# Performance work log

Measured on AMD Instinct MI355X. Metric: run time of the kernel, lower is better.

The kernel has to match this reference:

```python
import jax, jax.numpy as jnp
import numpy as np

B = 16384        # batch
P = 8            # num policies (experts)
D = 512          # latent dim
A = 64           # action dim
H = 1024         # hidden dim


def setup_inputs() -> dict:
    key = jax.random.key(0)
    ks = jax.random.split(key, 7)
    latents = jax.random.normal(ks[0], (B, D), dtype=jnp.float32)
    actions = jax.random.normal(ks[1], (B, A), dtype=jnp.float32)
    policy_indices = jax.random.randint(ks[2], (B,), 0, P, dtype=jnp.int64)
    # Per-policy 2-layer MLP params: concat(latent, action) -> hidden -> latent
    scale1 = 1.0 / np.sqrt(D + A)
    scale2 = 1.0 / np.sqrt(H)
    W1 = jax.random.normal(ks[3], (P, D + A, H), dtype=jnp.float32) * scale1
    b1 = jnp.zeros((P, H), dtype=jnp.float32)
    W2 = jax.random.normal(ks[4], (P, H, D), dtype=jnp.float32) * scale2
    b2 = jnp.zeros((P, D), dtype=jnp.float32)
    return {"latents": latents, "actions": actions, "policy_indices": policy_indices,
            "W1": W1, "b1": b1, "W2": W2, "b2": b2}


def reference(latents, actions, policy_indices, W1, b1, W2, b2):
    # Original: for each policy i, route rows with policy_indices == i through
    # that policy's dynamics model; scatter results back into next_latents.
    # Equivalent dense form: run all experts, then select per-row expert output.
    x = jnp.concatenate([latents, actions], axis=-1)          # [B, D+A]
    h = jax.nn.relu(jnp.einsum('bd,pdh->bph', x, W1) + b1)    # [B, P, H]
    y = jnp.einsum('bph,phd->bpd', h, W2) + b2                # [B, P, D]
    idx = policy_indices[:, None, None]                       # [B, 1, 1]
    next_latents = jnp.take_along_axis(y, idx, axis=1)[:, 0]  # [B, D]
    return next_latents
```

## Files before the change

kernel.cpp:

```cpp
#include <hip/hip_runtime.h>
#include <hip/hip_bf16.h>
#include <stdint.h>

#define B_SZ 16384
#define P_SZ 8
#define D_SZ 512
#define A_SZ 64
#define K1 576
#define H_SZ 1024
#define NSEG 64
#define MB_MAX 72
#define BPAD (B_SZ + P_SZ*256)
#define PREP_BLOCKS (BPAD * 72 / 256)
#define TRANS_BLOCKS (32 * 32 * 16)

typedef __bf16 bf16_t;
typedef __bf16 bf16x8 __attribute__((ext_vector_type(8)));
typedef float f32x4 __attribute__((ext_vector_type(4)));

__device__ __forceinline__ void glds16(const void* g, void* l) {
    __builtin_amdgcn_global_load_lds(
        (const __attribute__((address_space(1))) unsigned*)g,
        (__attribute__((address_space(3))) unsigned*)l, 16, 0, 0);
}


__global__ __launch_bounds__(256) void hist_block(const int* __restrict__ pol,
                                                  int* __restrict__ blockhist,
                                                  int* __restrict__ rowidx) {
    __shared__ int lc[P_SZ];
    int t = threadIdx.x;
    if (t < P_SZ) lc[t] = 0;
    __syncthreads();
    int gid = blockIdx.x * 256 + t;
    rowidx[gid] = -1;
    if (gid < BPAD - B_SZ) rowidx[B_SZ + gid] = -1;
    atomicAdd(&lc[pol[gid]], 1);
    __syncthreads();
    if (t < P_SZ) blockhist[blockIdx.x * P_SZ + t] = lc[t];
}

__global__ __launch_bounds__(64) void prefix_kernel(const int* __restrict__ blockhist,
                                                    int* __restrict__ counts,
                                                    int* __restrict__ cursors,
                                                    int* __restrict__ blk_p) {
    int t = threadIdx.x;
    if (t < P_SZ) {
        int s = 0;
        for (int b = 0; b < NSEG; ++b) s += blockhist[b * P_SZ + t];
        counts[t] = s;
    }
    __syncthreads();
    if (t == 0) {
        int run = 0;
        for (int p = 0; p < P_SZ; ++p) {
            cursors[p] = run;
            int nb = (counts[p] + 255) >> 8;
            for (int b = 0; b < nb; ++b) blk_p[(run >> 8) + b] = p;
            run += nb * 256;
        }
        for (int b = run >> 8; b < MB_MAX; ++b) blk_p[b] = -1;
    }
}

__global__ __launch_bounds__(256) void scatter_agg(const int* __restrict__ pol,
                                                   int* __restrict__ cursors,
                                                   int* __restrict__ rowidx) {
    __shared__ int lc[P_SZ], base_s[P_SZ];
    int t = threadIdx.x;
    if (t < P_SZ) lc[t] = 0;
    __syncthreads();
    int i = blockIdx.x * 256 + t;
    int p = pol[i];
    int lpos = atomicAdd(&lc[p], 1);
    __syncthreads();
    if (t < P_SZ) base_s[t] = atomicAdd(&cursors[t], lc[t]);
    __syncthreads();
    rowidx[base_s[p] + lpos] = i;
}


__global__ __launch_bounds__(256) void prep_all(const float* __restrict__ latents,
                                                const float* __restrict__ actions,
                                                const int* __restrict__ rowidx,
                                                const float* __restrict__ W1,
                                                const float* __restrict__ W2,
                                                bf16_t* __restrict__ xs,
                                                bf16_t* __restrict__ w1t,
                                                bf16_t* __restrict__ w2t) {
    int bx = blockIdx.x;
    int tid = threadIdx.x;
    if (bx < PREP_BLOCKS) {
        int idx = bx * 256 + tid;
        int s = idx / 72;
        int col = (idx - s * 72) * 8;
        int g = rowidx[s];
        bf16x8 o;
        if (g < 0) {
            o = (bf16x8){0,0,0,0,0,0,0,0};
        } else {
            const float* src;
            if (col < D_SZ) src = latents + (size_t)g * D_SZ + col;
            else            src = actions + (size_t)g * A_SZ + (col - D_SZ);
            f32x4 v0 = *(const f32x4*)src;
            f32x4 v1 = *(const f32x4*)(src + 4);
            o[0] = (bf16_t)v0[0]; o[1] = (bf16_t)v0[1]; o[2] = (bf16_t)v0[2]; o[3] = (bf16_t)v0[3];
            o[4] = (bf16_t)v1[0]; o[5] = (bf16_t)v1[1]; o[6] = (bf16_t)v1[2]; o[7] = (bf16_t)v1[3];
        }
        *(bf16x8*)(xs + (size_t)s * K1 + col) = o;
        return;
    }
    int tz = bx - PREP_BLOCKS;
    int z = tz >> 10;
    int rem = tz & 1023;
    int k0 = (rem & 31) * 32, n0 = (rem >> 5) * 32;
    int K = (z < P_SZ) ? K1 : H_SZ;
    int N = (z < P_SZ) ? H_SZ : D_SZ;
    if (k0 >= K || n0 >= N) return;
    int p = z & 7;
    const float* Wp = ((z < P_SZ) ? W1 : W2) + (size_t)p * K * N;
    bf16_t* WTp = ((z < P_SZ) ? w1t : w2t) + (size_t)p * N * K;
    __shared__ float ls[32][33];
#pragma unroll
    for (int e = 0; e < 4; ++e) {
        int idx = e * 256 + tid;
        int kk = idx >> 5, nn = idx & 31;
        ls[kk][nn] = Wp[(size_t)(k0 + kk) * N + n0 + nn];
    }
    __syncthreads();
#pragma unroll
    for (int e = 0; e < 2; ++e) {
        int idx = e * 256 + tid;
        int nn = idx >> 4, kp = (idx & 15) * 2;
        union { bf16_t h[2]; unsigned u; } pk;
        pk.h[0] = (bf16_t)ls[kp][nn];
        pk.h[1] = (bf16_t)ls[kp + 1][nn];
        *(unsigned*)&WTp[(size_t)(n0 + nn) * K + k0 + kp] = pk.u;
    }
}


__global__ __launch_bounds__(256, 2) void gemm1_kernel(
    const bf16_t* __restrict__ xs, const bf16_t* __restrict__ w1t,
    const float* __restrict__ b1, const int* __restrict__ blk_p,
    bf16_t* __restrict__ h) {

    const int p = blk_p[blockIdx.x];
    if (p < 0) return;
    const int m0 = blockIdx.x * 256;
    const int n0 = blockIdx.y * 128;

    __shared__ __align__(16) bf16_t As[256 * 32];
    __shared__ __align__(16) bf16_t Bs[128 * 32];

    const int tid = threadIdx.x;
    const int wave = tid >> 6, lane = tid & 63;

    const bf16_t* a_src[4]; bf16_t* a_dst[4];
#pragma unroll
    for (int i = 0; i < 4; ++i) {
        int c = (wave * 4 + i) * 64 + lane;
        int r = c >> 2;
        int kl = (c & 3) ^ ((r >> 1) & 3);
        a_src[i] = xs + (size_t)(m0 + r) * K1 + kl * 8;
        a_dst[i] = As + c * 8;
    }
    const bf16_t* b_src[2]; bf16_t* b_dst[2];
#pragma unroll
    for (int i = 0; i < 2; ++i) {
        int c = (wave * 2 + i) * 64 + lane;
        int r = c >> 2;
        int kl = (c & 3) ^ ((r >> 1) & 3);
        b_src[i] = w1t + ((size_t)p * H_SZ + n0 + r) * K1 + kl * 8;
        b_dst[i] = Bs + c * 8;
    }

    const int l16 = lane & 15, qd = lane >> 4;
    const int swz = (l16 >> 1) & 3;
    int aoff[4], boff[8];
#pragma unroll
    for (int i = 0; i < 4; ++i) aoff[i] = (wave * 64 + i * 16 + l16) * 32 + ((qd ^ swz) * 8);
#pragma unroll
    for (int j = 0; j < 8; ++j) boff[j] = (j * 16 + l16) * 32 + ((qd ^ swz) * 8);

    f32x4 acc[4][8];
#pragma unroll
    for (int i = 0; i < 4; ++i)
#pragma unroll
        for (int j = 0; j < 8; ++j)
            acc[i][j] = (f32x4){0.f, 0.f, 0.f, 0.f};

    for (int kt = 0; kt < K1; kt += 32) {
        __syncthreads();
#pragma unroll
        for (int i = 0; i < 4; ++i) glds16(a_src[i] + kt, a_dst[i]);
#pragma unroll
        for (int i = 0; i < 2; ++i) glds16(b_src[i] + kt, b_dst[i]);
        __syncthreads();
        bf16x8 af[4], bfv[8];
#pragma unroll
        for (int i = 0; i < 4; ++i) af[i] = *(const bf16x8*)(As + aoff[i]);
#pragma unroll
        for (int j = 0; j < 8; ++j) bfv[j] = *(const bf16x8*)(Bs + boff[j]);
#pragma unroll
        for (int i = 0; i < 4; ++i)
#pragma unroll
            for (int j = 0; j < 8; ++j)
                acc[i][j] = __builtin_amdgcn_mfma_f32_16x16x32_bf16(af[i], bfv[j], acc[i][j], 0, 0, 0);
    }

#pragma unroll
    for (int i = 0; i < 4; ++i) {
#pragma unroll
        for (int r = 0; r < 4; ++r) {
            int ml = wave * 64 + i * 16 + qd * 4 + r;
            size_t row = (size_t)(m0 + ml);
#pragma unroll
            for (int j = 0; j < 8; ++j) {
                int n = n0 + j * 16 + l16;
                float v = acc[i][j][r] + b1[p * H_SZ + n];
                h[row * H_SZ + n] = (bf16_t)fmaxf(v, 0.f);
            }
        }
    }
}

__global__ __launch_bounds__(256, 2) void gemm2_kernel(
    const bf16_t* __restrict__ h, const bf16_t* __restrict__ w2t,
    const float* __restrict__ b2, const int* __restrict__ blk_p,
    const int* __restrict__ rowidx, float* __restrict__ out) {

    const int p = blk_p[blockIdx.x];
    if (p < 0) return;
    const int m0 = blockIdx.x * 256;
    const int n0 = blockIdx.y * 64;

    __shared__ __align__(16) bf16_t As[256 * 32];
    __shared__ __align__(16) bf16_t Bs[64 * 32];

    const int tid = threadIdx.x;
    const int wave = tid >> 6, lane = tid & 63;

    const bf16_t* a_src[4]; bf16_t* a_dst[4];
#pragma unroll
    for (int i = 0; i < 4; ++i) {
        int c = (wave * 4 + i) * 64 + lane;
        int r = c >> 2;
        int kl = (c & 3) ^ ((r >> 1) & 3);
        a_src[i] = h + (size_t)(m0 + r) * H_SZ + kl * 8;
        a_dst[i] = As + c * 8;
    }
    const bf16_t* b_src0; bf16_t* b_dst0;
    {
        int c = wave * 64 + lane;
        int r = c >> 2;
        int kl = (c & 3) ^ ((r >> 1) & 3);
        b_src0 = w2t + ((size_t)p * D_SZ + n0 + r) * H_SZ + kl * 8;
        b_dst0 = Bs + c * 8;
    }

    const int l16 = lane & 15, qd = lane >> 4;
    const int swz = (l16 >> 1) & 3;
    int aoff[4], boff[4];
#pragma unroll
    for (int i = 0; i < 4; ++i) aoff[i] = (wave * 64 + i * 16 + l16) * 32 + ((qd ^ swz) * 8);
#pragma unroll
    for (int j = 0; j < 4; ++j) boff[j] = (j * 16 + l16) * 32 + ((qd ^ swz) * 8);

    f32x4 acc[4][4];
#pragma unroll
    for (int i = 0; i < 4; ++i)
#pragma unroll
        for (int j = 0; j < 4; ++j)
            acc[i][j] = (f32x4){0.f, 0.f, 0.f, 0.f};

    for (int kt = 0; kt < H_SZ; kt += 32) {
        __syncthreads();
#pragma unroll
        for (int i = 0; i < 4; ++i) glds16(a_src[i] + kt, a_dst[i]);
        glds16(b_src0 + kt, b_dst0);
        __syncthreads();
        bf16x8 af[4], bfv[4];
#pragma unroll
        for (int i = 0; i < 4; ++i) af[i] = *(const bf16x8*)(As + aoff[i]);
#pragma unroll
        for (int j = 0; j < 4; ++j) bfv[j] = *(const bf16x8*)(Bs + boff[j]);
#pragma unroll
        for (int i = 0; i < 4; ++i)
#pragma unroll
            for (int j = 0; j < 4; ++j)
                acc[i][j] = __builtin_amdgcn_mfma_f32_16x16x32_bf16(af[i], bfv[j], acc[i][j], 0, 0, 0);
    }

#pragma unroll
    for (int i = 0; i < 4; ++i) {
#pragma unroll
        for (int r = 0; r < 4; ++r) {
            int ml = wave * 64 + i * 16 + qd * 4 + r;
            int g = rowidx[m0 + ml];
            if (g >= 0) {
                size_t orow = (size_t)g * D_SZ;
#pragma unroll
                for (int j = 0; j < 4; ++j) {
                    int n = n0 + j * 16 + l16;
                    out[orow + n] = acc[i][j][r] + b2[p * D_SZ + n];
                }
            }
        }
    }
}


extern "C" void kernel_launch(void* const* d_in, const int* in_sizes, int n_in,
                              void* d_out, int out_size, void* d_ws, size_t ws_size,
                              hipStream_t stream) {
    const float* latents = (const float*)d_in[0];
    const float* actions = (const float*)d_in[1];
    const int*   pol     = (const int*)d_in[2];
    const float* W1      = (const float*)d_in[3];
    const float* b1      = (const float*)d_in[4];
    const float* W2      = (const float*)d_in[5];
    const float* b2      = (const float*)d_in[6];
    float* out = (float*)d_out;

    char* ws = (char*)d_ws;
    int* counts    = (int*)ws;
    int* cursors   = counts + P_SZ;
    int* blk_p     = cursors + P_SZ;
    int* blockhist = blk_p + MB_MAX;
    int* rowidx    = blockhist + NSEG * P_SZ;
    size_t pos = ((size_t)(2 * P_SZ + MB_MAX + NSEG * P_SZ + BPAD) * sizeof(int) + 255) & ~(size_t)255;
    bf16_t* xs  = (bf16_t*)(ws + pos);  pos += (size_t)BPAD * K1 * 2;
    bf16_t* hbuf= (bf16_t*)(ws + pos);  pos += (size_t)BPAD * H_SZ * 2;
    bf16_t* w1t = (bf16_t*)(ws + pos);  pos += (size_t)P_SZ * H_SZ * K1 * 2;
    bf16_t* w2t = (bf16_t*)(ws + pos);  pos += (size_t)P_SZ * D_SZ * H_SZ * 2;

    hist_block<<<NSEG, 256, 0, stream>>>(pol, blockhist, rowidx);
    prefix_kernel<<<1, 64, 0, stream>>>(blockhist, counts, cursors, blk_p);
    scatter_agg<<<NSEG, 256, 0, stream>>>(pol, cursors, rowidx);
    prep_all<<<PREP_BLOCKS + TRANS_BLOCKS, 256, 0, stream>>>(
        latents, actions, rowidx, W1, W2, xs, w1t, w2t);
    gemm1_kernel<<<dim3(MB_MAX, H_SZ / 128), 256, 0, stream>>>(xs, w1t, b1, blk_p, hbuf);
    gemm2_kernel<<<dim3(MB_MAX, D_SZ / 64), 256, 0, stream>>>(hbuf, w2t, b2, blk_p, rowidx, out);
}
```

Measured before the change: 210.8 us.

## Double-buffer LDS tiles in both GEMMs and vectorize weight transpose loads

Both grouped GEMM kernels now keep two LDS buffers for the A and B tiles. The next K-tile is issued with global_load_lds before the current one is consumed, leaving a single barrier per iteration. The goal is to hide global-load latency behind the MFMA work. Occupancy hints are raised to 3 and 4 blocks per CU to go with the larger LDS footprint. The prep transpose now reads weights as float4 instead of scalars. The compiler may still insert full vmcnt waits before the LDS reads, which would limit the overlap, and the higher launch bounds constrain register allocation.

```diff
diff --git a/kernel.cpp b/kernel.cpp
--- a/kernel.cpp
+++ b/kernel.cpp
@@ -121,11 +121,13 @@
     const float* Wp = ((z < P_SZ) ? W1 : W2) + (size_t)p * K * N;
     bf16_t* WTp = ((z < P_SZ) ? w1t : w2t) + (size_t)p * N * K;
     __shared__ float ls[32][33];
-#pragma unroll
-    for (int e = 0; e < 4; ++e) {
-        int idx = e * 256 + tid;
-        int kk = idx >> 5, nn = idx & 31;
-        ls[kk][nn] = Wp[(size_t)(k0 + kk) * N + n0 + nn];
+    {
+        int kk = tid >> 3, nn = (tid & 7) * 4;
+        f32x4 v = *(const f32x4*)&Wp[(size_t)(k0 + kk) * N + n0 + nn];
+        ls[kk][nn]     = v[0];
+        ls[kk][nn + 1] = v[1];
+        ls[kk][nn + 2] = v[2];
+        ls[kk][nn + 3] = v[3];
     }
     __syncthreads();
 #pragma unroll
@@ -140,7 +142,7 @@
 }
 
 
-__global__ __launch_bounds__(256, 2) void gemm1_kernel(
+__global__ __launch_bounds__(256, 3) void gemm1_kernel(
     const bf16_t* __restrict__ xs, const bf16_t* __restrict__ w1t,
     const float* __restrict__ b1, const int* __restrict__ blk_p,
     bf16_t* __restrict__ h) {
@@ -150,8 +152,10 @@
     const int m0 = blockIdx.x * 256;
     const int n0 = blockIdx.y * 128;
 
-    __shared__ __align__(16) bf16_t As[256 * 32];
-    __shared__ __align__(16) bf16_t Bs[128 * 32];
+    constexpr int AE = 256 * 32;
+    constexpr int BE = 128 * 32;
+    __shared__ __align__(16) bf16_t As[2 * AE];
+    __shared__ __align__(16) bf16_t Bs[2 * BE];
 
     const int tid = threadIdx.x;
     const int wave = tid >> 6, lane = tid & 63;
@@ -175,6 +179,11 @@
         b_dst[i] = Bs + c * 8;
     }
 
+#pragma unroll
+    for (int i = 0; i < 4; ++i) glds16(a_src[i], a_dst[i]);
+#pragma unroll
+    for (int i = 0; i < 2; ++i) glds16(b_src[i], b_dst[i]);
+
     const int l16 = lane & 15, qd = lane >> 4;
     const int swz = (l16 >> 1) & 3;
     int aoff[4], boff[8];
@@ -190,18 +199,25 @@
         for (int j = 0; j < 8; ++j)
             acc[i][j] = (f32x4){0.f, 0.f, 0.f, 0.f};
 
-    for (int kt = 0; kt < K1; kt += 32) {
+    constexpr int NT = K1 / 32;
+    for (int t = 0; t < NT; ++t) {
         __syncthreads();
-#pragma unroll
-        for (int i = 0; i < 4; ++i) glds16(a_src[i] + kt, a_dst[i]);
-#pragma unroll
-        for (int i = 0; i < 2; ++i) glds16(b_src[i] + kt, b_dst[i]);
-        __syncthreads();
+        const int nxt = t + 1;
+        if (nxt < NT) {
+            const int po = (nxt & 1) ? AE : 0;
+            const int pb = (nxt & 1) ? BE : 0;
+#pragma unroll
+            for (int i = 0; i < 4; ++i) glds16(a_src[i] + nxt * 32, a_dst[i] + po);
+#pragma unroll
+            for (int i = 0; i < 2; ++i) glds16(b_src[i] + nxt * 32, b_dst[i] + pb);
+        }
+        const int co = (t & 1) ? AE : 0;
+        const int cb = (t & 1) ? BE : 0;
         bf16x8 af[4], bfv[8];
 #pragma unroll
-        for (int i = 0; i < 4; ++i) af[i] = *(const bf16x8*)(As + aoff[i]);
-#pragma unroll
-        for (int j = 0; j < 8; ++j) bfv[j] = *(const bf16x8*)(Bs + boff[j]);
+        for (int i = 0; i < 4; ++i) af[i] = *(const bf16x8*)(As + co + aoff[i]);
+#pragma unroll
+        for (int j = 0; j < 8; ++j) bfv[j] = *(const bf16x8*)(Bs + cb + boff[j]);
 #pragma unroll
         for (int i = 0; i < 4; ++i)
 #pragma unroll
@@ -225,7 +241,7 @@
     }
 }
 
-__global__ __launch_bounds__(256, 2) void gemm2_kernel(
+__global__ __launch_bounds__(256, 4) void gemm2_kernel(
     const bf16_t* __restrict__ h, const bf16_t* __restrict__ w2t,
     const float* __restrict__ b2, const int* __restrict__ blk_p,
     const int* __restrict__ rowidx, float* __restrict__ out) {
@@ -235,8 +251,10 @@
     const int m0 = blockIdx.x * 256;
     const int n0 = blockIdx.y * 64;
 
-    __shared__ __align__(16) bf16_t As[256 * 32];
-    __shared__ __align__(16) bf16_t Bs[64 * 32];
+    constexpr int AE = 256 * 32;
+    constexpr int BE = 64 * 32;
+    __shared__ __align__(16) bf16_t As[2 * AE];
+    __shared__ __align__(16) bf16_t Bs[2 * BE];
 
     const int tid = threadIdx.x;
     const int wave = tid >> 6, lane = tid & 63;
@@ -259,6 +277,10 @@
         b_dst0 = Bs + c * 8;
     }
 
+#pragma unroll
+    for (int i = 0; i < 4; ++i) glds16(a_src[i], a_dst[i]);
+    glds16(b_src0, b_dst0);
+
     const int l16 = lane & 15, qd = lane >> 4;
     const int swz = (l16 >> 1) & 3;
     int aoff[4], boff[4];
@@ -274,17 +296,24 @@
         for (int j = 0; j < 4; ++j)
             acc[i][j] = (f32x4){0.f, 0.f, 0.f, 0.f};
 
-    for (int kt = 0; kt < H_SZ; kt += 32) {
+    constexpr int NT = H_SZ / 32;
+    for (int t = 0; t < NT; ++t) {
         __syncthreads();
-#pragma unroll
-        for (int i = 0; i < 4; ++i) glds16(a_src[i] + kt, a_dst[i]);
-        glds16(b_src0 + kt, b_dst0);
-        __syncthreads();
+        const int nxt = t + 1;
+        if (nxt < NT) {
+            const int po = (nxt & 1) ? AE : 0;
+            const int pb = (nxt & 1) ? BE : 0;
+#pragma unroll
+            for (int i = 0; i < 4; ++i) glds16(a_src[i] + nxt * 32, a_dst[i] + po);
+            glds16(b_src0 + nxt * 32, b_dst0 + pb);
+        }
+        const int co = (t & 1) ? AE : 0;
+        const int cb = (t & 1) ? BE : 0;
         bf16x8 af[4], bfv[4];
 #pragma unroll
-        for (int i = 0; i < 4; ++i) af[i] = *(const bf16x8*)(As + aoff[i]);
-#pragma unroll
-        for (int j = 0; j < 4; ++j) bfv[j] = *(const bf16x8*)(Bs + boff[j]);
+        for (int i = 0; i < 4; ++i) af[i] = *(const bf16x8*)(As + co + aoff[i]);
+#pragma unroll
+        for (int j = 0; j < 4; ++j) bfv[j] = *(const bf16x8*)(Bs + cb + boff[j]);
 #pragma unroll
         for (int i = 0; i < 4; ++i)
 #pragma unroll
```

New measurement: 240.6 us. 1.14x slower.

## Triple-buffer LDS tiles in both GEMMs and vectorize weight transpose loads

Applied to the files above, without the earlier changes.

Both grouped GEMM kernels now keep three LDS stages. They prefetch two k-tiles ahead with direct global-to-LDS loads, use vmcnt waits plus a single barrier per iteration, and rotate buffer offsets, so memory latency overlaps with MFMA work instead of being exposed by two full syncs per tile. The weight transpose prep kernel also loads fp32 weights as float4 vectors instead of scalars. The larger LDS footprint (up to about 72KB per block in gemm1) may reduce occupancy at the requested two blocks per CU. The hand-tuned vmcnt counts must also match the number of outstanding loads.

```diff
diff --git a/kernel.cpp b/kernel.cpp
--- a/kernel.cpp
+++ b/kernel.cpp
@@ -121,11 +121,13 @@
     const float* Wp = ((z < P_SZ) ? W1 : W2) + (size_t)p * K * N;
     bf16_t* WTp = ((z < P_SZ) ? w1t : w2t) + (size_t)p * N * K;
     __shared__ float ls[32][33];
-#pragma unroll
-    for (int e = 0; e < 4; ++e) {
-        int idx = e * 256 + tid;
-        int kk = idx >> 5, nn = idx & 31;
-        ls[kk][nn] = Wp[(size_t)(k0 + kk) * N + n0 + nn];
+    {
+        int kk = tid >> 3, nn = (tid & 7) * 4;
+        f32x4 v = *(const f32x4*)&Wp[(size_t)(k0 + kk) * N + n0 + nn];
+        ls[kk][nn]     = v[0];
+        ls[kk][nn + 1] = v[1];
+        ls[kk][nn + 2] = v[2];
+        ls[kk][nn + 3] = v[3];
     }
     __syncthreads();
 #pragma unroll
@@ -150,30 +152,42 @@
     const int m0 = blockIdx.x * 256;
     const int n0 = blockIdx.y * 128;
 
-    __shared__ __align__(16) bf16_t As[256 * 32];
-    __shared__ __align__(16) bf16_t Bs[128 * 32];
+    constexpr int AE = 256 * 32;
+    constexpr int BE = 128 * 32;
+    __shared__ __align__(16) bf16_t As[3 * AE];
+    __shared__ __align__(16) bf16_t Bs[3 * BE];
 
     const int tid = threadIdx.x;
     const int wave = tid >> 6, lane = tid & 63;
 
-    const bf16_t* a_src[4]; bf16_t* a_dst[4];
+    const bf16_t* a_src[4]; int a_slot[4];
 #pragma unroll
     for (int i = 0; i < 4; ++i) {
         int c = (wave * 4 + i) * 64 + lane;
         int r = c >> 2;
         int kl = (c & 3) ^ ((r >> 1) & 3);
         a_src[i] = xs + (size_t)(m0 + r) * K1 + kl * 8;
-        a_dst[i] = As + c * 8;
-    }
-    const bf16_t* b_src[2]; bf16_t* b_dst[2];
+        a_slot[i] = c * 8;
+    }
+    const bf16_t* b_src[2]; int b_slot[2];
 #pragma unroll
     for (int i = 0; i < 2; ++i) {
         int c = (wave * 2 + i) * 64 + lane;
         int r = c >> 2;
         int kl = (c & 3) ^ ((r >> 1) & 3);
         b_src[i] = w1t + ((size_t)p * H_SZ + n0 + r) * K1 + kl * 8;
-        b_dst[i] = Bs + c * 8;
-    }
+        b_slot[i] = c * 8;
+    }
+
+    auto stage = [&](int kt, int oA, int oB) {
+#pragma unroll
+        for (int i = 0; i < 4; ++i) glds16(a_src[i] + kt, As + oA + a_slot[i]);
+#pragma unroll
+        for (int i = 0; i < 2; ++i) glds16(b_src[i] + kt, Bs + oB + b_slot[i]);
+    };
+
+    stage(0, 0, 0);
+    stage(32, AE, BE);
 
     const int l16 = lane & 15, qd = lane >> 4;
     const int swz = (l16 >> 1) & 3;
@@ -190,23 +204,27 @@
         for (int j = 0; j < 8; ++j)
             acc[i][j] = (f32x4){0.f, 0.f, 0.f, 0.f};
 
-    for (int kt = 0; kt < K1; kt += 32) {
-        __syncthreads();
-#pragma unroll
-        for (int i = 0; i < 4; ++i) glds16(a_src[i] + kt, a_dst[i]);
-#pragma unroll
-        for (int i = 0; i < 2; ++i) glds16(b_src[i] + kt, b_dst[i]);
-        __syncthreads();
+    int cA0 = 0, cA1 = AE, cA2 = 2 * AE;
+    int cB0 = 0, cB1 = BE, cB2 = 2 * BE;
+
+    constexpr int NT = K1 / 32;
+    for (int t = 0; t < NT; ++t) {
+        if (t < NT - 1) asm volatile("s_waitcnt vmcnt(6)" ::: "memory");
+        else            asm volatile("s_waitcnt vmcnt(0)" ::: "memory");
+        __builtin_amdgcn_s_barrier();
+        if (t + 2 < NT) stage((t + 2) * 32, cA2, cB2);
         bf16x8 af[4], bfv[8];
 #pragma unroll
-        for (int i = 0; i < 4; ++i) af[i] = *(const bf16x8*)(As + aoff[i]);
-#pragma unroll
-        for (int j = 0; j < 8; ++j) bfv[j] = *(const bf16x8*)(Bs + boff[j]);
+        for (int i = 0; i < 4; ++i) af[i] = *(const bf16x8*)(As + cA0 + aoff[i]);
+#pragma unroll
+        for (int j = 0; j < 8; ++j) bfv[j] = *(const bf16x8*)(Bs + cB0 + boff[j]);
 #pragma unroll
         for (int i = 0; i < 4; ++i)
 #pragma unroll
             for (int j = 0; j < 8; ++j)
                 acc[i][j] = __builtin_amdgcn_mfma_f32_16x16x32_bf16(af[i], bfv[j], acc[i][j], 0, 0, 0);
+        int ta = cA0; cA0 = cA1; cA1 = cA2; cA2 = ta;
+        int tb = cB0; cB0 = cB1; cB1 = cB2; cB2 = tb;
     }
 
 #pragma unroll
@@ -235,29 +253,40 @@
     const int m0 = blockIdx.x * 256;
     const int n0 = blockIdx.y * 64;
 
-    __shared__ __align__(16) bf16_t As[256 * 32];
-    __shared__ __align__(16) bf16_t Bs[64 * 32];
+    constexpr int AE = 256 * 32;
+    constexpr int BE = 64 * 32;
+    __shared__ __align__(16) bf16_t As[3 * AE];
+    __shared__ __align__(16) bf16_t Bs[3 * BE];
 
     const int tid = threadIdx.x;
     const int wave = tid >> 6, lane = tid & 63;
 
-    const bf16_t* a_src[4]; bf16_t* a_dst[4];
+    const bf16_t* a_src[4]; int a_slot[4];
 #pragma unroll
     for (int i = 0; i < 4; ++i) {
         int c = (wave * 4 + i) * 64 + lane;
         int r = c >> 2;
         int kl = (c & 3) ^ ((r >> 1) & 3);
         a_src[i] = h + (size_t)(m0 + r) * H_SZ + kl * 8;
-        a_dst[i] = As + c * 8;
-    }
-    const bf16_t* b_src0; bf16_t* b_dst0;
+        a_slot[i] = c * 8;
+    }
+    const bf16_t* b_src0; int b_slot0;
     {
         int c = wave * 64 + lane;
         int r = c >> 2;
         int kl = (c & 3) ^ ((r >> 1) & 3);
         b_src0 = w2t + ((size_t)p * D_SZ + n0 + r) * H_SZ + kl * 8;
-        b_dst0 = Bs + c * 8;
-    }
+        b_slot0 = c * 8;
+    }
+
+    auto stage = [&](int kt, int oA, int oB) {
+#pragma unroll
+        for (int i = 0; i < 4; ++i) glds16(a_src[i] + kt, As + oA + a_slot[i]);
+        glds16(b_src0 + kt, Bs + oB + b_slot0);
+    };
+
+    stage(0, 0, 0);
+    stage(32, AE, BE);
 
     const int l16 = lane & 15, qd = lane >> 4;
     const int swz = (l16 >> 1) & 3;
@@ -274,22 +303,27 @@
         for (int j = 0; j < 4; ++j)
             acc[i][j] = (f32x4){0.f, 0.f, 0.f, 0.f};
 
-    for (int kt = 0; kt < H_SZ; kt += 32) {
-        __syncthreads();
-#pragma unroll
-        for (int i = 0; i < 4; ++i) glds16(a_src[i] + kt, a_dst[i]);
-        glds16(b_src0 + kt, b_dst0);
-        __syncthreads();
+    int cA0 = 0, cA1 = AE, cA2 = 2 * AE;
+    int cB0 = 0, cB1 = BE, cB2 = 2 * BE;
+
+    constexpr int NT = H_SZ / 32;
+    for (int t = 0; t < NT; ++t) {
+        if (t < NT - 1) asm volatile("s_waitcnt vmcnt(5)" ::: "memory");
+        else            asm volatile("s_waitcnt vmcnt(0)" ::: "memory");
+        __builtin_amdgcn_s_barrier();
+        if (t + 2 < NT) stage((t + 2) * 32, cA2, cB2);
         bf16x8 af[4], bfv[4];
 #pragma unroll
-        for (int i = 0; i < 4; ++i) af[i] = *(const bf16x8*)(As + aoff[i]);
-#pragma unroll
-        for (int j = 0; j < 4; ++j) bfv[j] = *(const bf16x8*)(Bs + boff[j]);
+        for (int i = 0; i < 4; ++i) af[i] = *(const bf16x8*)(As + cA0 + aoff[i]);
+#pragma unroll
+        for (int j = 0; j < 4; ++j) bfv[j] = *(const bf16x8*)(Bs + cB0 + boff[j]);
 #pragma unroll
         for (int i = 0; i < 4; ++i)
 #pragma unroll
             for (int j = 0; j < 4; ++j)
                 acc[i][j] = __builtin_amdgcn_mfma_f32_16x16x32_bf16(af[i], bfv[j], acc[i][j], 0, 0, 0);
+        int ta = cA0; cA0 = cA1; cA1 = cA2; cA2 = ta;
+        int tb = cB0; cB0 = cB1; cB1 = cB2; cB2 = tb;
     }
 
 #pragma unroll
```

Result: slower. 234.1 us (+11.0%).
